# Kernel tuning notes

Hardware: AMD Instinct MI355X
Metric: run time of the kernel (lower is better)

## Reference

```python
import jax, jax.numpy as jnp
import numpy as np

N_ATOM = 100000
N_BOND = 400000
N_GLOBAL = 5000
IN = 128
OUT = 128
HEADS = 2
NEG_SLOPE = 0.2
BN_EPS = 1e-5


def setup_inputs() -> dict:
    key = jax.random.key(0)
    ks = jax.random.split(key, 12)
    atom_feats = jax.random.normal(ks[0], (N_ATOM, IN), jnp.float32)
    bond_feats = jax.random.normal(ks[1], (N_BOND, IN), jnp.float32)
    global_feats = jax.random.normal(ks[2], (N_GLOBAL, IN), jnp.float32)
    W_atom = jax.random.normal(ks[3], (IN, OUT * HEADS), jnp.float32) * 0.05
    W_bond = jax.random.normal(ks[4], (IN, OUT * HEADS), jnp.float32) * 0.05
    W_global = jax.random.normal(ks[5], (IN, OUT * HEADS), jnp.float32) * 0.05
    attn_l = jax.random.normal(ks[6], (1, HEADS, OUT), jnp.float32) * 0.1
    attn_r = jax.random.normal(ks[7], (1, HEADS, OUT), jnp.float32) * 0.1
    bn_gamma = jnp.ones((OUT,), jnp.float32)
    bn_beta = jnp.zeros((OUT,), jnp.float32)
    bond_src = jax.random.randint(ks[8], (N_BOND,), 0, N_ATOM, jnp.int32)
    # ensure every atom appears as a bond destination at least once (DGL-like semantics)
    bond_dst = jnp.concatenate([
        jnp.arange(N_ATOM, dtype=jnp.int32),
        jax.random.randint(ks[9], (N_BOND - N_ATOM,), 0, N_ATOM, jnp.int32),
    ])
    g2a_src = jax.random.randint(ks[10], (N_ATOM,), 0, N_GLOBAL, jnp.int32)
    return dict(atom_feats=atom_feats, bond_feats=bond_feats, global_feats=global_feats,
                W_atom=W_atom, W_bond=W_bond, W_global=W_global,
                attn_l=attn_l, attn_r=attn_r, bn_gamma=bn_gamma, bn_beta=bn_beta,
                bond_src=bond_src, bond_dst=bond_dst, g2a_src=g2a_src)


def _fwd(atom_feats, bond_feats, global_feats, W_atom, W_bond, W_global,
         attn_l, attn_r, bn_gamma, bn_beta, bond_src, bond_dst, g2a_src):
    lrelu = lambda x: jax.nn.leaky_relu(x, NEG_SLOPE)
    # projections -> [*, H, D]
    h = (atom_feats @ W_atom).reshape(-1, HEADS, OUT)      # [N,H,D]
    e = (bond_feats @ W_bond).reshape(-1, HEADS, OUT)      # [E,H,D]
    u = (global_feats @ W_global).reshape(-1, HEADS, OUT)  # [G,H,D]
    er = (h * attn_r).sum(-1)    # [N,H]
    el_h = (h * attn_l).sum(-1)  # [N,H]
    el_e = (e * attn_l).sum(-1)  # [E,H]
    el_u = (u * attn_l).sum(-1)  # [G,H]
    er_dst = er[bond_dst]                      # [E,H]
    eh = lrelu(el_h[bond_src] + er_dst)        # bond: u_add_v
    ee = lrelu(el_e + er_dst)                  # bond: e_add_v
    eu = lrelu(el_u[g2a_src] + er)             # g2a: u_add_v (dst = arange(N))
    # numerically-stable edge softmax over both edge types per destination atom
    emax_b = jax.ops.segment_max(jnp.maximum(eh, ee), bond_dst, num_segments=N_ATOM)
    emax = jnp.maximum(emax_b, eu)             # [N,H]
    eh = jnp.exp(eh - emax[bond_dst])
    ee = jnp.exp(ee - emax[bond_dst])
    eu = jnp.exp(eu - emax)
    esum = jax.ops.segment_sum(eh + ee, bond_dst, num_segments=N_ATOM) + eu  # [N,H]
    esum_dst = esum[bond_dst]
    alpha_h = eh / esum_dst    # [E,H]
    alpha_e = ee / esum_dst
    alpha_u = eu / esum        # [N,H]
    msg = h[bond_src] * alpha_h[:, :, None] + e * alpha_e[:, :, None]  # [E,H,D]
    out = jax.ops.segment_sum(msg, bond_dst, num_segments=N_ATOM)
    out = out + u[g2a_src] * alpha_u[:, :, None]   # [N,H,D]
    hN = out.mean(axis=1)                           # mean over heads -> [N,D]
    # BatchNorm1d (training-mode batch stats, biased var)
    mean = hN.mean(axis=0)
    var = ((hN - mean) ** 2).mean(axis=0)
    hN = (hN - mean) * jax.lax.rsqrt(var + BN_EPS) * bn_gamma + bn_beta
    return jax.nn.relu(hN)


def reference(atom_feats, bond_feats, global_feats, W_atom, W_bond, W_global,
              attn_l, attn_r, bn_gamma, bn_beta, bond_src, bond_dst, g2a_src):
    return _fwd(atom_feats, bond_feats, global_feats, W_atom, W_bond, W_global,
                attn_l, attn_r, bn_gamma, bn_beta, bond_src, bond_dst, g2a_src)
```

## Files before the change

### kernel.cpp

```cpp
#include <hip/hip_runtime.h>
#include <hip/hip_bf16.h>

#define NA 100000
#define NB 400000
#define NG 5000
#define NEG 0.2f
#define KDIM 512
#define CAP 32
#define FG_BLKS 782
#define KSC_BLKS 7891

typedef __attribute__((ext_vector_type(8))) short bf16x8;
typedef __attribute__((ext_vector_type(8))) unsigned short u16x8;
typedef __attribute__((ext_vector_type(4))) float f32x4;

__device__ __forceinline__ float lrelu(float x){ return x > 0.f ? x : NEG*x; }
__device__ __forceinline__ unsigned short f2bf(float f){
  unsigned u = __float_as_uint(f);
  u = (u + 0x7FFFu + ((u>>16)&1u)) >> 16;
  return (unsigned short)u;
}
__device__ __forceinline__ float bf2f(unsigned short s){
  return __uint_as_float(((unsigned)s) << 16);
}
__device__ __forceinline__ ushort2 pk2(float x, float y){
  __hip_bfloat162 t = __float22bfloat162_rn(make_float2(x, y));
  return *reinterpret_cast<ushort2*>(&t);
}

__global__ void kW(const float* __restrict__ Wa, const float* __restrict__ Wb,
                   const float* __restrict__ Wg, const float* __restrict__ glob,
                   const float* __restrict__ al, const float* __restrict__ ar,
                   unsigned short* wTa, unsigned short* wTb, unsigned short* wTu,
                   unsigned short* WcT, unsigned short* P){
  int blk = blockIdx.x;
  int tid = threadIdx.x;
  if (blk == 0){
    int k = tid >> 1, h = tid & 1;
    const float* wa = Wa + k*256 + h*128;
    const float* wb = Wb + k*256 + h*128;
    const float* wg = Wg + k*256 + h*128;
    const float* pl = al + h*128;
    const float* pr = ar + h*128;
    float sa=0.f, sra=0.f, se=0.f, su=0.f;
    for (int d=0; d<128; ++d){
      float L = pl[d], R = pr[d];
      sa  += wa[d]*L;  sra += wa[d]*R;
      se  += wb[d]*L;  su  += wg[d]*L;
    }
    wTa[h*128 + k]     = f2bf(sa);
    wTa[(2+h)*128 + k] = f2bf(sra);
    wTb[h*128 + k]     = f2bf(se);
    wTu[h*128 + k]     = f2bf(su);
    for (int idx = tid; idx < 14*128; idx += 256){
      int c = 2 + (idx >> 7), k2 = idx & 127;
      wTb[c*128 + k2] = 0;
      wTu[c*128 + k2] = 0;
      if (c >= 4) wTa[c*128 + k2] = 0;
    }
  } else if (blk <= 256){
    int idx = (blk-1)*256 + tid;
    int c = idx / KDIM, j = idx % KDIM;
    int part = j >> 7, k = j & 127;
    const float* W = (part < 2) ? Wa : Wb;
    int h = part & 1;
    WcT[(size_t)c*KDIM + j] = f2bf(0.5f * W[k*256 + h*128 + c]);
  } else {
    __shared__ float gl[8][128];
    int g0 = (blk-257)*8;
    #pragma unroll
    for (int r=0;r<4;++r){
      int idx = r*256+tid;
      gl[idx>>7][idx&127] = glob[(size_t)(g0 + (idx>>7))*128 + (idx&127)];
    }
    __syncthreads();
    float acc[8];
    #pragma unroll
    for (int g=0;g<8;++g) acc[g]=0.f;
    for (int k=0;k<128;++k){
      float wv = Wg[k*256 + tid];
      #pragma unroll
      for (int g=0;g<8;++g) acc[g] += gl[g][k]*wv;
    }
    #pragma unroll
    for (int g=0;g<8;++g)
      P[(size_t)(g0+g)*256 + tid] = f2bf(0.5f*acc[g]);
  }
}

__global__ __launch_bounds__(256) void kSC(
    const float* __restrict__ atom, const float* __restrict__ bond,
    const float* __restrict__ glob,
    const unsigned short* __restrict__ wTa, const unsigned short* __restrict__ wTb,
    const unsigned short* __restrict__ wTu,
    float* __restrict__ el_h, float* __restrict__ er,
    float* __restrict__ el_e, float* __restrict__ el_u,
    unsigned short* __restrict__ atomB, unsigned short* __restrict__ bondB){
  __shared__ unsigned short lds[4][16*128];
  const int wid = threadIdx.x >> 6;
  const int l = threadIdx.x & 63;
  const long rowbase = ((long)blockIdx.x*4 + wid) * 16;

  const float* feats; const unsigned short* wT; unsigned short* fb;
  long r0; long nrows; int type;
  if (rowbase < NA){            feats = atom; wT = wTa; fb = atomB; r0 = rowbase;          nrows = NA; type = 0; }
  else if (rowbase < NA+NB){    feats = bond; wT = wTb; fb = bondB; r0 = rowbase-NA;       nrows = NB; type = 1; }
  else {                        feats = glob; wT = wTu; fb = nullptr; r0 = rowbase-(NA+NB); nrows = NG; type = 2; }

  bf16x8 bfrag[4];
  #pragma unroll
  for (int kk=0;kk<4;++kk)
    bfrag[kk] = *reinterpret_cast<const bf16x8*>(wT + (size_t)(l&15)*128 + kk*32 + (l>>4)*8);

  unsigned short* wlds = lds[wid];
  const int j = l & 15;
  const int rl0 = l >> 4;
  #pragma unroll
  for (int i=0;i<4;++i){
    int rl = rl0 + i*4;
    long gr = r0 + rl;
    long grc = gr < nrows ? gr : (nrows-1);
    const float* src = feats + grc*128 + j*8;
    float4 x0 = *reinterpret_cast<const float4*>(src);
    float4 x1 = *reinterpret_cast<const float4*>(src+4);
    u16x8 w;
    ushort2 c0 = pk2(x0.x, x0.y), c1 = pk2(x0.z, x0.w);
    ushort2 c2 = pk2(x1.x, x1.y), c3 = pk2(x1.z, x1.w);
    w[0]=c0.x; w[1]=c0.y; w[2]=c1.x; w[3]=c1.y;
    w[4]=c2.x; w[5]=c2.y; w[6]=c3.x; w[7]=c3.y;
    *reinterpret_cast<u16x8*>(&wlds[rl*128 + ((j ^ (rl&7))*8)]) = w;
    if (fb && gr < nrows)
      *reinterpret_cast<u16x8*>(fb + grc*128 + j*8) = w;
  }
  __syncthreads();

  f32x4 acc = (f32x4){0.f,0.f,0.f,0.f};
  const int arow = l & 15;
  #pragma unroll
  for (int kk=0;kk<4;++kk){
    int ch = (kk*4 + (l>>4)) ^ (arow & 7);
    bf16x8 a = *reinterpret_cast<const bf16x8*>(&wlds[arow*128 + ch*8]);
    acc = __builtin_amdgcn_mfma_f32_16x16x32_bf16(a, bfrag[kk], acc, 0, 0, 0);
  }

  const int col = l & 15;
  if (col < 4 && (type == 0 || col < 2)){
    #pragma unroll
    for (int i=0;i<4;++i){
      long gr = r0 + (l>>4)*4 + i;
      if (gr < nrows){
        float v = acc[i];
        if (type == 0){
          if (col < 2) el_h[2*gr + col] = v;
          else         er[2*gr + col-2] = v;
        } else if (type == 1){
          el_e[2*gr + col] = v;
        } else {
          el_u[2*gr + col] = v;
        }
      }
    }
  }
}

__global__ void k4_edgeexp(const int* __restrict__ bsrc, const int* __restrict__ bdst,
                           const float* __restrict__ el_h, const float* __restrict__ er,
                           const float* __restrict__ el_e,
                           int2* __restrict__ slot_bs, float4* __restrict__ slot_e,
                           int* __restrict__ cursor, float* __restrict__ esum){
  int b = blockIdx.x*256 + threadIdx.x;
  if (b >= NB) return;
  int s = bsrc[b], d = bdst[b];
  float2 elh = *reinterpret_cast<const float2*>(&el_h[2*s]);
  float2 erd = *reinterpret_cast<const float2*>(&er[2*d]);
  float2 ele = *reinterpret_cast<const float2*>(&el_e[2*b]);
  float a0 = __expf(lrelu(elh.x + erd.x));
  float a1 = __expf(lrelu(elh.y + erd.y));
  float b0 = __expf(lrelu(ele.x + erd.x));
  float b1 = __expf(lrelu(ele.y + erd.y));
  int pos = atomicAdd(&cursor[d], 1);
  if (pos < CAP){
    slot_bs[(size_t)d*CAP + pos] = make_int2(b, s);
    slot_e [(size_t)d*CAP + pos] = make_float4(a0, a1, b0, b1);
  }
  atomicAdd(&esum[2*d],   a0 + b0);
  atomicAdd(&esum[2*d+1], a1 + b1);
}

__global__ __launch_bounds__(512, 4) void kFG(
    const unsigned short* __restrict__ atomB,
    const unsigned short* __restrict__ bondB,
    const int2* __restrict__ slot_bs, const float4* __restrict__ slot_e,
    const int* __restrict__ cursor, const float* __restrict__ esum,
    const float* __restrict__ el_u, const float* __restrict__ er,
    const int* __restrict__ g2a,
    const unsigned short* __restrict__ WcT,
    const unsigned short* __restrict__ P,
    float* __restrict__ out, float* __restrict__ colsum, float* __restrict__ colsq){
  __shared__ unsigned short XA[128*256];
  __shared__ float au_s[128][2];
  const int tid = threadIdx.x;
  const int l  = tid & 63;
  const int li = tid & 15;
  const int gid = tid >> 4;
  const int w = tid >> 6;
  const int wr = w >> 2, wc = w & 3;
  const int gb = l & 48;
  const int n0 = blockIdx.x * 128;

  f32x4 acc[4][2];
  #pragma unroll
  for (int m=0;m<4;++m)
    #pragma unroll
    for (int nf=0;nf<2;++nf) acc[m][nf] = (f32x4){0.f,0.f,0.f,0.f};

  auto agg = [&](int phase){
    for (int t=0; t<4; ++t){
      int ln = gid + t*32;
      int n = n0 + ln;
      float a0[8], a1[8];
      #pragma unroll
      for (int k2=0;k2<8;++k2){ a0[k2]=0.f; a1[k2]=0.f; }
      int cc = 0; float iv0=0.f, iv1=0.f;
      if (n < NA){
        cc = cursor[n]; cc = cc > CAP ? CAP : cc;
        int g = g2a[n];
        float2 elu = *reinterpret_cast<const float2*>(&el_u[2*g]);
        float2 ern = *reinterpret_cast<const float2*>(&er[2*n]);
        float u0 = __expf(lrelu(elu.x + ern.x));
        float u1 = __expf(lrelu(elu.y + ern.y));
        iv0 = 1.f/(esum[2*n]   + u0);
        iv1 = 1.f/(esum[2*n+1] + u1);
        if (phase==0 && li==0){ au_s[ln][0]=u0*iv0; au_s[ln][1]=u1*iv1; }
      }
      int idxA=0, idxB=0; float w0A=0.f,w1A=0.f,w0B=0.f,w1B=0.f;
      if (li < cc){
        int2 bs = slot_bs[(size_t)n*CAP + li];
        float4 e = slot_e[(size_t)n*CAP + li];
        idxA = phase ? bs.x : bs.y;
        w0A = phase ? e.z : e.x;
        w1A = phase ? e.w : e.y;
      }
      if (li+16 < cc){
        int2 bs = slot_bs[(size_t)n*CAP + li+16];
        float4 e = slot_e[(size_t)n*CAP + li+16];
        idxB = phase ? bs.x : bs.y;
        w0B = phase ? e.z : e.x;
        w1B = phase ? e.w : e.y;
      }
      const unsigned short* tbl = phase ? bondB : atomB;
      if (cc > 0){
        const int last = cc - 1;
        #define IDXJ(J) ({ int _jj = (J) <= last ? (J) : last; \
                           int _sl = gb + (_jj & 15); \
                           (_jj < 16) ? __shfl(idxA, _sl) : __shfl(idxB, _sl); })
        u16x8 x0 = *reinterpret_cast<const u16x8*>(tbl + (size_t)IDXJ(0)*128 + li*8);
        u16x8 x1 = *reinterpret_cast<const u16x8*>(tbl + (size_t)IDXJ(1)*128 + li*8);
        u16x8 x2 = *reinterpret_cast<const u16x8*>(tbl + (size_t)IDXJ(2)*128 + li*8);
        u16x8 x3 = *reinterpret_cast<const u16x8*>(tbl + (size_t)IDXJ(3)*128 + li*8);
        for (int j0 = 0; j0 < cc; j0 += 4){
          u16x8 y0=x0, y1=x1, y2=x2, y3=x3;
          x0 = *reinterpret_cast<const u16x8*>(tbl + (size_t)IDXJ(j0+4)*128 + li*8);
          x1 = *reinterpret_cast<const u16x8*>(tbl + (size_t)IDXJ(j0+5)*128 + li*8);
          x2 = *reinterpret_cast<const u16x8*>(tbl + (size_t)IDXJ(j0+6)*128 + li*8);
          x3 = *reinterpret_cast<const u16x8*>(tbl + (size_t)IDXJ(j0+7)*128 + li*8);
          #define CONSUME(YY, JJ) { \
            int _j = j0 + (JJ); \
            int _jc = _j <= last ? _j : last; \
            int _sl = gb + (_jc & 15); \
            float _w0 = (_jc < 16) ? __shfl(w0A, _sl) : __shfl(w0B, _sl); \
            float _w1 = (_jc < 16) ? __shfl(w1A, _sl) : __shfl(w1B, _sl); \
            float _c0 = (_j <= last) ? _w0*iv0 : 0.f; \
            float _c1 = (_j <= last) ? _w1*iv1 : 0.f; \
            _Pragma("unroll") \
            for (int k2=0;k2<8;++k2){ \
              float _v = bf2f((YY)[k2]); \
              a0[k2] += _c0*_v; a1[k2] += _c1*_v; \
            } }
          CONSUME(y0, 0)
          CONSUME(y1, 1)
          CONSUME(y2, 2)
          CONSUME(y3, 3)
          #undef CONSUME
        }
        #undef IDXJ
      }
      u16x8 o0, o1;
      #pragma unroll
      for (int k2=0;k2<8;++k2){ o0[k2]=f2bf(a0[k2]); o1[k2]=f2bf(a1[k2]); }
      *reinterpret_cast<u16x8*>(&XA[ln*256 + ((li   ) ^ (ln&7))*8]) = o0;
      *reinterpret_cast<u16x8*>(&XA[ln*256 + ((16+li) ^ (ln&7))*8]) = o1;
    }
  };

  auto gemm = [&](int phase){
    #pragma unroll
    for (int ks=0; ks<8; ++ks){
      bf16x8 av[4], bv[2];
      #pragma unroll
      for (int m=0;m<4;++m){
        int row = wr*64 + m*16 + (l&15);
        int ch = (ks*4 + (l>>4)) ^ (row&7);
        av[m] = *reinterpret_cast<const bf16x8*>(&XA[row*256 + ch*8]);
      }
      #pragma unroll
      for (int nf=0;nf<2;++nf){
        int col = wc*32 + nf*16 + (l&15);
        bv[nf] = *reinterpret_cast<const bf16x8*>(
            WcT + (size_t)col*KDIM + phase*256 + ks*32 + (l>>4)*8);
      }
      #pragma unroll
      for (int m=0;m<4;++m)
        #pragma unroll
        for (int nf=0;nf<2;++nf)
          acc[m][nf] = __builtin_amdgcn_mfma_f32_16x16x32_bf16(av[m], bv[nf], acc[m][nf], 0, 0, 0);
    }
  };

  agg(0);
  __syncthreads();
  gemm(0);
  __syncthreads();
  agg(1);
  __syncthreads();
  gemm(1);

  float s[2] = {0.f,0.f};
  float q[2] = {0.f,0.f};
  #pragma unroll
  for (int m=0;m<4;++m){
    #pragma unroll
    for (int i=0;i<4;++i){
      int row_l = wr*64 + m*16 + (l>>4)*4 + i;
      size_t row = (size_t)n0 + row_l;
      if (row < NA){
        float aux = au_s[row_l][0], auy = au_s[row_l][1];
        int g = g2a[row];
        const unsigned short* Pg = P + (size_t)g*256;
        #pragma unroll
        for (int nf=0;nf<2;++nf){
          int col = wc*32 + nf*16 + (l&15);
          float v = acc[m][nf][i] + aux*bf2f(Pg[col]) + auy*bf2f(Pg[128+col]);
          out[row*128 + col] = v;
          s[nf] += v; q[nf] += v*v;
        }
      }
    }
  }
  #pragma unroll
  for (int nf=0;nf<2;++nf){
    int col = wc*32 + nf*16 + (l&15);
    float sv = s[nf], qv = q[nf];
    sv += __shfl_xor(sv, 16); sv += __shfl_xor(sv, 32);
    qv += __shfl_xor(qv, 16); qv += __shfl_xor(qv, 32);
    if (l < 16){
      atomicAdd(&colsum[col], sv);
      atomicAdd(&colsq[col],  qv);
    }
  }
}

__global__ __launch_bounds__(256) void k11_bnrelu(float* __restrict__ out,
                            const float* __restrict__ colsum, const float* __restrict__ colsq,
                            const float* __restrict__ gamma, const float* __restrict__ beta){
  __shared__ float sc[128], sh[128];
  int t = threadIdx.x;
  if (t < 128){
    float mean = colsum[t] / (float)NA;
    float var = fmaxf(colsq[t] / (float)NA - mean*mean, 0.f);
    float s = gamma[t] * rsqrtf(var + 1e-5f);
    sc[t] = s;
    sh[t] = beta[t] - mean*s;
  }
  __syncthreads();
  int i = blockIdx.x*256 + t;
  float4 v = reinterpret_cast<float4*>(out)[i];
  int c0 = (i*4) & 127;
  v.x = fmaxf(0.f, v.x*sc[c0]   + sh[c0]);
  v.y = fmaxf(0.f, v.y*sc[c0+1] + sh[c0+1]);
  v.z = fmaxf(0.f, v.z*sc[c0+2] + sh[c0+2]);
  v.w = fmaxf(0.f, v.w*sc[c0+3] + sh[c0+3]);
  reinterpret_cast<float4*>(out)[i] = v;
}

extern "C" void kernel_launch(void* const* d_in, const int* in_sizes, int n_in,
                              void* d_out, int out_size, void* d_ws, size_t ws_size,
                              hipStream_t stream) {
  const float* atom = (const float*)d_in[0];
  const float* bond = (const float*)d_in[1];
  const float* glob = (const float*)d_in[2];
  const float* Wa   = (const float*)d_in[3];
  const float* Wb   = (const float*)d_in[4];
  const float* Wg   = (const float*)d_in[5];
  const float* al   = (const float*)d_in[6];
  const float* ar   = (const float*)d_in[7];
  const float* gamma= (const float*)d_in[8];
  const float* beta = (const float*)d_in[9];
  const int* bsrc   = (const int*)d_in[10];
  const int* bdst   = (const int*)d_in[11];
  const int* g2a    = (const int*)d_in[12];
  float* out = (float*)d_out;

  char* base = (char*)d_ws;
  size_t off = 0;
  auto carve = [&](size_t bytes)->void*{
    void* p = base + off;
    off = (off + bytes + 255) & ~(size_t)255;
    return p;
  };
  unsigned short* wTa = (unsigned short*)carve((size_t)16*128*2);
  unsigned short* wTb = (unsigned short*)carve((size_t)16*128*2);
  unsigned short* wTu = (unsigned short*)carve((size_t)16*128*2);
  unsigned short* WcT = (unsigned short*)carve((size_t)128*KDIM*2);
  unsigned short* P   = (unsigned short*)carve((size_t)NG*256*2);
  float* el_h = (float*)carve((size_t)NA*2*4);
  float* er   = (float*)carve((size_t)NA*2*4);
  float* el_e = (float*)carve((size_t)NB*2*4);
  float* el_u = (float*)carve((size_t)NG*2*4);
  char* zr = (char*)carve((size_t)NA*2*4 + (size_t)NA*4 + 256*4);
  float* esum   = (float*)(zr);
  int*   cursor = (int*)(zr + (size_t)NA*2*4);
  float* colsum = (float*)(zr + (size_t)NA*2*4 + (size_t)NA*4);
  float* colsq  = colsum + 128;
  size_t zbytes = (size_t)NA*2*4 + (size_t)NA*4 + 256*4;
  int2*   slot_bs = (int2*)carve((size_t)NA*CAP*8);
  float4* slot_e  = (float4*)carve((size_t)NA*CAP*16);
  unsigned short* atomB = (unsigned short*)carve((size_t)NA*128*2);
  unsigned short* bondB = (unsigned short*)carve((size_t)NB*128*2);

  hipMemsetAsync(zr, 0, zbytes, stream);

  kW<<<882, 256, 0, stream>>>(Wa, Wb, Wg, glob, al, ar, wTa, wTb, wTu, WcT, P);

  kSC<<<KSC_BLKS, 256, 0, stream>>>(atom, bond, glob, wTa, wTb, wTu,
                                    el_h, er, el_e, el_u, atomB, bondB);

  k4_edgeexp<<<1563, 256, 0, stream>>>(bsrc, bdst, el_h, er, el_e,
                                       slot_bs, slot_e, cursor, esum);

  kFG<<<FG_BLKS, 512, 0, stream>>>(atomB, bondB, slot_bs, slot_e, cursor, esum,
                                   el_u, er, g2a, WcT, P, out, colsum, colsq);

  k11_bnrelu<<<12500, 256, 0, stream>>>(out, colsum, colsq, gamma, beta);
}
```

Measured before the change: 314.6 us.

## Halve kFG tile to 64 atoms, precompute per-atom softmax terms in a separate kernel

Adds a kPre kernel that computes the per-atom inverse softmax denominators, global-node attention weights and clamped neighbor counts into compact arrays. kFG now handles 64 atoms per block instead of 128, doubling the block count, halving LDS, and raising the occupancy hint to 6. Slot metadata is loaded once up front for both phases, the GEMM is remapped to one M-fragment by four N-fragments per wave, and column statistics are reduced in LDS before the atomics. This trades an extra launch and extra global traffic for more parallelism and latency hiding in the gather-bound fused kernel.

After: 409.5 us. +30.2%, slower.

```diff
diff --git a/kernel.cpp b/kernel.cpp
--- a/kernel.cpp
+++ b/kernel.cpp
@@ -7,7 +7,7 @@
 #define NEG 0.2f
 #define KDIM 512
 #define CAP 32
-#define FG_BLKS 782
+#define FG_BLKS 1563
 #define KSC_BLKS 7891
 
 typedef __attribute__((ext_vector_type(8))) short bf16x8;
@@ -187,176 +187,181 @@
   atomicAdd(&esum[2*d+1], a1 + b1);
 }
 
-__global__ __launch_bounds__(512, 4) void kFG(
+__global__ void kPre(const int* __restrict__ cursor, const float* __restrict__ esum,
+                     const float* __restrict__ el_u, const float* __restrict__ er,
+                     const int* __restrict__ g2a,
+                     float4* __restrict__ recF, int* __restrict__ recC){
+  int n = blockIdx.x*256 + threadIdx.x;
+  if (n >= NA) return;
+  int cc = cursor[n]; cc = cc > CAP ? CAP : cc;
+  int g = g2a[n];
+  float2 elu = *reinterpret_cast<const float2*>(&el_u[2*g]);
+  float2 ern = *reinterpret_cast<const float2*>(&er[2*n]);
+  float u0 = __expf(lrelu(elu.x + ern.x));
+  float u1 = __expf(lrelu(elu.y + ern.y));
+  float iv0 = 1.f/(esum[2*n]   + u0);
+  float iv1 = 1.f/(esum[2*n+1] + u1);
+  recF[n] = make_float4(iv0, iv1, u0*iv0, u1*iv1);
+  recC[n] = cc;
+}
+
+__global__ __launch_bounds__(512, 6) void kFG(
     const unsigned short* __restrict__ atomB,
     const unsigned short* __restrict__ bondB,
     const int2* __restrict__ slot_bs, const float4* __restrict__ slot_e,
-    const int* __restrict__ cursor, const float* __restrict__ esum,
-    const float* __restrict__ el_u, const float* __restrict__ er,
+    const float4* __restrict__ recF, const int* __restrict__ recC,
     const int* __restrict__ g2a,
     const unsigned short* __restrict__ WcT,
     const unsigned short* __restrict__ P,
     float* __restrict__ out, float* __restrict__ colsum, float* __restrict__ colsq){
-  __shared__ unsigned short XA[128*256];
-  __shared__ float au_s[128][2];
+  __shared__ unsigned short XA[64*256];
   const int tid = threadIdx.x;
   const int l  = tid & 63;
   const int li = tid & 15;
   const int gid = tid >> 4;
   const int w = tid >> 6;
-  const int wr = w >> 2, wc = w & 3;
+  const int wr = w >> 1, wc = w & 1;
   const int gb = l & 48;
-  const int n0 = blockIdx.x * 128;
-
-  f32x4 acc[4][2];
-  #pragma unroll
-  for (int m=0;m<4;++m)
-    #pragma unroll
-    for (int nf=0;nf<2;++nf) acc[m][nf] = (f32x4){0.f,0.f,0.f,0.f};
-
-  auto agg = [&](int phase){
-    for (int t=0; t<4; ++t){
-      int ln = gid + t*32;
-      int n = n0 + ln;
-      float a0[8], a1[8];
+  const int n0 = blockIdx.x * 64;
+
+  const int nA = n0 + gid;
+  const int nB = n0 + gid + 32;
+  int ccA = 0, ccB = 0;
+  float4 rA = make_float4(0.f,0.f,0.f,0.f), rB = make_float4(0.f,0.f,0.f,0.f);
+  if (nA < NA){ ccA = recC[nA]; rA = recF[nA]; }
+  if (nB < NA){ ccB = recC[nB]; rB = recF[nB]; }
+  int2 sA0 = make_int2(0,0), sA1 = make_int2(0,0);
+  int2 sB0 = make_int2(0,0), sB1 = make_int2(0,0);
+  float4 eA0 = make_float4(0.f,0.f,0.f,0.f), eA1 = eA0, eB0 = eA0, eB1 = eA0;
+  if (li < ccA){    sA0 = slot_bs[(size_t)nA*CAP + li];    eA0 = slot_e[(size_t)nA*CAP + li]; }
+  if (li+16 < ccA){ sA1 = slot_bs[(size_t)nA*CAP + li+16]; eA1 = slot_e[(size_t)nA*CAP + li+16]; }
+  if (li < ccB){    sB0 = slot_bs[(size_t)nB*CAP + li];    eB0 = slot_e[(size_t)nB*CAP + li]; }
+  if (li+16 < ccB){ sB1 = slot_bs[(size_t)nB*CAP + li+16]; eB1 = slot_e[(size_t)nB*CAP + li+16]; }
+
+  f32x4 acc[4];
+  #pragma unroll
+  for (int nf=0;nf<4;++nf) acc[nf] = (f32x4){0.f,0.f,0.f,0.f};
+
+  auto agg_atom = [&](int phase, int ln, int cc, float iv0, float iv1,
+                      int2 s0, int2 s1, const float4& e0, const float4& e1){
+    float a0[8], a1[8];
+    #pragma unroll
+    for (int k2=0;k2<8;++k2){ a0[k2]=0.f; a1[k2]=0.f; }
+    int idx0 = phase ? s0.x : s0.y;
+    int idx1 = phase ? s1.x : s1.y;
+    float w00 = phase ? e0.z : e0.x, w10 = phase ? e0.w : e0.y;
+    float w01 = phase ? e1.z : e1.x, w11 = phase ? e1.w : e1.y;
+    const unsigned short* tbl = phase ? bondB : atomB;
+    if (cc > 0){
+      const int last = cc - 1;
+      #define IDXJ(J) ({ int _jj = (J) <= last ? (J) : last; \
+                         int _sl = gb + (_jj & 15); \
+                         (_jj < 16) ? __shfl(idx0, _sl) : __shfl(idx1, _sl); })
+      u16x8 x0 = *reinterpret_cast<const u16x8*>(tbl + (size_t)IDXJ(0)*128 + li*8);
+      u16x8 x1 = *reinterpret_cast<const u16x8*>(tbl + (size_t)IDXJ(1)*128 + li*8);
+      u16x8 x2 = *reinterpret_cast<const u16x8*>(tbl + (size_t)IDXJ(2)*128 + li*8);
+      u16x8 x3 = *reinterpret_cast<const u16x8*>(tbl + (size_t)IDXJ(3)*128 + li*8);
+      for (int j0 = 0; j0 < cc; j0 += 4){
+        u16x8 y0=x0, y1=x1, y2=x2, y3=x3;
+        x0 = *reinterpret_cast<const u16x8*>(tbl + (size_t)IDXJ(j0+4)*128 + li*8);
+        x1 = *reinterpret_cast<const u16x8*>(tbl + (size_t)IDXJ(j0+5)*128 + li*8);
+        x2 = *reinterpret_cast<const u16x8*>(tbl + (size_t)IDXJ(j0+6)*128 + li*8);
+        x3 = *reinterpret_cast<const u16x8*>(tbl + (size_t)IDXJ(j0+7)*128 + li*8);
+        #define CONSUME(YY, JJ) { \
+          int _j = j0 + (JJ); \
+          int _jc = _j <= last ? _j : last; \
+          int _sl = gb + (_jc & 15); \
+          float _w0 = (_jc < 16) ? __shfl(w00, _sl) : __shfl(w01, _sl); \
+          float _w1 = (_jc < 16) ? __shfl(w10, _sl) : __shfl(w11, _sl); \
+          float _c0 = (_j <= last) ? _w0*iv0 : 0.f; \
+          float _c1 = (_j <= last) ? _w1*iv1 : 0.f; \
+          _Pragma("unroll") \
+          for (int k2=0;k2<8;++k2){ \
+            float _v = bf2f((YY)[k2]); \
+            a0[k2] += _c0*_v; a1[k2] += _c1*_v; \
+          } }
+        CONSUME(y0, 0)
+        CONSUME(y1, 1)
+        CONSUME(y2, 2)
+        CONSUME(y3, 3)
+        #undef CONSUME
+      }
+      #undef IDXJ
+    }
+    u16x8 o0, o1;
+    #pragma unroll
+    for (int k2=0;k2<8;++k2){ o0[k2]=f2bf(a0[k2]); o1[k2]=f2bf(a1[k2]); }
+    *reinterpret_cast<u16x8*>(&XA[ln*256 + ((li   ) ^ (ln&7))*8]) = o0;
+    *reinterpret_cast<u16x8*>(&XA[ln*256 + ((16+li) ^ (ln&7))*8]) = o1;
+  };
+
+  auto gemm = [&](int phase){
+    #pragma unroll
+    for (int ks=0; ks<8; ++ks){
+      int row = wr*16 + (l & 15);
+      int ch = (ks*4 + (l>>4)) ^ (row & 7);
+      bf16x8 av = *reinterpret_cast<const bf16x8*>(&XA[row*256 + ch*8]);
       #pragma unroll
-      for (int k2=0;k2<8;++k2){ a0[k2]=0.f; a1[k2]=0.f; }
-      int cc = 0; float iv0=0.f, iv1=0.f;
-      if (n < NA){
-        cc = cursor[n]; cc = cc > CAP ? CAP : cc;
-        int g = g2a[n];
-        float2 elu = *reinterpret_cast<const float2*>(&el_u[2*g]);
-        float2 ern = *reinterpret_cast<const float2*>(&er[2*n]);
-        float u0 = __expf(lrelu(elu.x + ern.x));
-        float u1 = __expf(lrelu(elu.y + ern.y));
-        iv0 = 1.f/(esum[2*n]   + u0);
-        iv1 = 1.f/(esum[2*n+1] + u1);
-        if (phase==0 && li==0){ au_s[ln][0]=u0*iv0; au_s[ln][1]=u1*iv1; }
+      for (int nf=0;nf<4;++nf){
+        int col = wc*64 + nf*16 + (l & 15);
+        bf16x8 bv = *reinterpret_cast<const bf16x8*>(
+            WcT + (size_t)col*KDIM + phase*256 + ks*32 + (l>>4)*8);
+        acc[nf] = __builtin_amdgcn_mfma_f32_16x16x32_bf16(av, bv, acc[nf], 0, 0, 0);
       }
-      int idxA=0, idxB=0; float w0A=0.f,w1A=0.f,w0B=0.f,w1B=0.f;
-      if (li < cc){
-        int2 bs = slot_bs[(size_t)n*CAP + li];
-        float4 e = slot_e[(size_t)n*CAP + li];
-        idxA = phase ? bs.x : bs.y;
-        w0A = phase ? e.z : e.x;
-        w1A = phase ? e.w : e.y;
+    }
+  };
+
+  agg_atom(0, gid,    ccA, rA.x, rA.y, sA0, sA1, eA0, eA1);
+  agg_atom(0, gid+32, ccB, rB.x, rB.y, sB0, sB1, eB0, eB1);
+  __syncthreads();
+  gemm(0);
+  __syncthreads();
+  agg_atom(1, gid,    ccA, rA.x, rA.y, sA0, sA1, eA0, eA1);
+  agg_atom(1, gid+32, ccB, rB.x, rB.y, sB0, sB1, eB0, eB1);
+  __syncthreads();
+  gemm(1);
+
+  float s[4] = {0.f,0.f,0.f,0.f};
+  float q[4] = {0.f,0.f,0.f,0.f};
+  #pragma unroll
+  for (int i=0;i<4;++i){
+    int row_l = wr*16 + (l>>4)*4 + i;
+    size_t row = (size_t)n0 + row_l;
+    if (row < NA){
+      float4 rec = recF[row];
+      int g = g2a[row];
+      const unsigned short* Pg = P + (size_t)g*256;
+      #pragma unroll
+      for (int nf=0;nf<4;++nf){
+        int col = wc*64 + nf*16 + (l&15);
+        float v = acc[nf][i] + rec.z*bf2f(Pg[col]) + rec.w*bf2f(Pg[128+col]);
+        out[row*128 + col] = v;
+        s[nf] += v; q[nf] += v*v;
       }
-      if (li+16 < cc){
-        int2 bs = slot_bs[(size_t)n*CAP + li+16];
-        float4 e = slot_e[(size_t)n*CAP + li+16];
-        idxB = phase ? bs.x : bs.y;
-        w0B = phase ? e.z : e.x;
-        w1B = phase ? e.w : e.y;
-      }
-      const unsigned short* tbl = phase ? bondB : atomB;
-      if (cc > 0){
-        const int last = cc - 1;
-        #define IDXJ(J) ({ int _jj = (J) <= last ? (J) : last; \
-                           int _sl = gb + (_jj & 15); \
-                           (_jj < 16) ? __shfl(idxA, _sl) : __shfl(idxB, _sl); })
-        u16x8 x0 = *reinterpret_cast<const u16x8*>(tbl + (size_t)IDXJ(0)*128 + li*8);
-        u16x8 x1 = *reinterpret_cast<const u16x8*>(tbl + (size_t)IDXJ(1)*128 + li*8);
-        u16x8 x2 = *reinterpret_cast<const u16x8*>(tbl + (size_t)IDXJ(2)*128 + li*8);
-        u16x8 x3 = *reinterpret_cast<const u16x8*>(tbl + (size_t)IDXJ(3)*128 + li*8);
-        for (int j0 = 0; j0 < cc; j0 += 4){
-          u16x8 y0=x0, y1=x1, y2=x2, y3=x3;
-          x0 = *reinterpret_cast<const u16x8*>(tbl + (size_t)IDXJ(j0+4)*128 + li*8);
-          x1 = *reinterpret_cast<const u16x8*>(tbl + (size_t)IDXJ(j0+5)*128 + li*8);
-          x2 = *reinterpret_cast<const u16x8*>(tbl + (size_t)IDXJ(j0+6)*128 + li*8);
-          x3 = *reinterpret_cast<const u16x8*>(tbl + (size_t)IDXJ(j0+7)*128 + li*8);
-          #define CONSUME(YY, JJ) { \
-            int _j = j0 + (JJ); \
-            int _jc = _j <= last ? _j : last; \
-            int _sl = gb + (_jc & 15); \
-            float _w0 = (_jc < 16) ? __shfl(w0A, _sl) : __shfl(w0B, _sl); \
-            float _w1 = (_jc < 16) ? __shfl(w1A, _sl) : __shfl(w1B, _sl); \
-            float _c0 = (_j <= last) ? _w0*iv0 : 0.f; \
-            float _c1 = (_j <= last) ? _w1*iv1 : 0.f; \
-            _Pragma("unroll") \
-            for (int k2=0;k2<8;++k2){ \
-              float _v = bf2f((YY)[k2]); \
-              a0[k2] += _c0*_v; a1[k2] += _c1*_v; \
-            } }
-          CONSUME(y0, 0)
-          CONSUME(y1, 1)
-          CONSUME(y2, 2)
-          CONSUME(y3, 3)
-          #undef CONSUME
-        }
-        #undef IDXJ
-      }
-      u16x8 o0, o1;
-      #pragma unroll
-      for (int k2=0;k2<8;++k2){ o0[k2]=f2bf(a0[k2]); o1[k2]=f2bf(a1[k2]); }
-      *reinterpret_cast<u16x8*>(&XA[ln*256 + ((li   ) ^ (ln&7))*8]) = o0;
-      *reinterpret_cast<u16x8*>(&XA[ln*256 + ((16+li) ^ (ln&7))*8]) = o1;
-    }
-  };
-
-  auto gemm = [&](int phase){
-    #pragma unroll
-    for (int ks=0; ks<8; ++ks){
-      bf16x8 av[4], bv[2];
-      #pragma unroll
-      for (int m=0;m<4;++m){
-        int row = wr*64 + m*16 + (l&15);
-        int ch = (ks*4 + (l>>4)) ^ (row&7);
-        av[m] = *reinterpret_cast<const bf16x8*>(&XA[row*256 + ch*8]);
-      }
-      #pragma unroll
-      for (int nf=0;nf<2;++nf){
-        int col = wc*32 + nf*16 + (l&15);
-        bv[nf] = *reinterpret_cast<const bf16x8*>(
-            WcT + (size_t)col*KDIM + phase*256 + ks*32 + (l>>4)*8);
-      }
-      #pragma unroll
-      for (int m=0;m<4;++m)
-        #pragma unroll
-        for (int nf=0;nf<2;++nf)
-          acc[m][nf] = __builtin_amdgcn_mfma_f32_16x16x32_bf16(av[m], bv[nf], acc[m][nf], 0, 0, 0);
-    }
-  };
-
-  agg(0);
-  __syncthreads();
-  gemm(0);
-  __syncthreads();
-  agg(1);
-  __syncthreads();
-  gemm(1);
-
-  float s[2] = {0.f,0.f};
-  float q[2] = {0.f,0.f};
-  #pragma unroll
-  for (int m=0;m<4;++m){
-    #pragma unroll
-    for (int i=0;i<4;++i){
-      int row_l = wr*64 + m*16 + (l>>4)*4 + i;
-      size_t row = (size_t)n0 + row_l;
-      if (row < NA){
-        float aux = au_s[row_l][0], auy = au_s[row_l][1];
-        int g = g2a[row];
-        const unsigned short* Pg = P + (size_t)g*256;
-        #pragma unroll
-        for (int nf=0;nf<2;++nf){
-          int col = wc*32 + nf*16 + (l&15);
-          float v = acc[m][nf][i] + aux*bf2f(Pg[col]) + auy*bf2f(Pg[128+col]);
-          out[row*128 + col] = v;
-          s[nf] += v; q[nf] += v*v;
-        }
-      }
-    }
-  }
-  #pragma unroll
-  for (int nf=0;nf<2;++nf){
-    int col = wc*32 + nf*16 + (l&15);
-    float sv = s[nf], qv = q[nf];
-    sv += __shfl_xor(sv, 16); sv += __shfl_xor(sv, 32);
-    qv += __shfl_xor(qv, 16); qv += __shfl_xor(qv, 32);
-    if (l < 16){
-      atomicAdd(&colsum[col], sv);
-      atomicAdd(&colsq[col],  qv);
-    }
+    }
+  }
+  #pragma unroll
+  for (int nf=0;nf<4;++nf){
+    s[nf] += __shfl_xor(s[nf], 16); s[nf] += __shfl_xor(s[nf], 32);
+    q[nf] += __shfl_xor(q[nf], 16); q[nf] += __shfl_xor(q[nf], 32);
+  }
+  float* red = reinterpret_cast<float*>(XA);
+  __syncthreads();
+  if (l < 16){
+    #pragma unroll
+    for (int nf=0;nf<4;++nf){
+      red[      w*64 + nf*16 + li] = s[nf];
+      red[512 + w*64 + nf*16 + li] = q[nf];
+    }
+  }
+  __syncthreads();
+  if (tid < 256){
+    int col = tid & 127, h = tid >> 7;
+    int wcb = col >> 6, c6 = col & 63;
+    float v = 0.f;
+    #pragma unroll
+    for (int k=0;k<4;++k) v += red[h*512 + (wcb + 2*k)*64 + c6];
+    atomicAdd((h ? colsq : colsum) + col, v);
   }
 }
 
@@ -417,6 +422,8 @@
   float* er   = (float*)carve((size_t)NA*2*4);
   float* el_e = (float*)carve((size_t)NB*2*4);
   float* el_u = (float*)carve((size_t)NG*2*4);
+  float4* recF = (float4*)carve((size_t)NA*16);
+  int*    recC = (int*)carve((size_t)NA*4);
   char* zr = (char*)carve((size_t)NA*2*4 + (size_t)NA*4 + 256*4);
   float* esum   = (float*)(zr);
   int*   cursor = (int*)(zr + (size_t)NA*2*4);
@@ -438,8 +445,10 @@
   k4_edgeexp<<<1563, 256, 0, stream>>>(bsrc, bdst, el_h, er, el_e,
                                        slot_bs, slot_e, cursor, esum);
 
-  kFG<<<FG_BLKS, 512, 0, stream>>>(atomB, bondB, slot_bs, slot_e, cursor, esum,
-                                   el_u, er, g2a, WcT, P, out, colsum, colsq);
+  kPre<<<391, 256, 0, stream>>>(cursor, esum, el_u, er, g2a, recF, recC);
+
+  kFG<<<FG_BLKS, 512, 0, stream>>>(atomB, bondB, slot_bs, slot_e, recF, recC,
+                                   g2a, WcT, P, out, colsum, colsq);
 
   k11_bnrelu<<<12500, 256, 0, stream>>>(out, colsum, colsq, gamma, beta);
 }
```
